# Kernel tuning notes

Measured on AMD Instinct MI355X. Metric: run time of the kernel, lower is better.

## Reference

```python
import jax, jax.numpy as jnp
import numpy as np

B, N, E, D = 128, 100, 100, 64
LAYERS = 2
ALPHA = 0.2  # LeakyReLU negative slope
NEG = -9e15


def leaky_relu(x):
    return jnp.where(x >= 0, x, ALPHA * x)


def setup_inputs() -> dict:
    key = jax.random.key(0)
    ks = jax.random.split(key, 10)
    stdv = 1.0 / np.sqrt(D)
    u = lambda k, shp: jax.random.uniform(k, shp, jnp.float32, -stdv, stdv)
    hidden = jax.random.normal(ks[0], (B, N, D), jnp.float32)
    H = jax.random.randint(ks[1], (B, N, E), 0, 4).astype(jnp.float32)
    s_c = jax.random.normal(ks[2], (B, 1, D), jnp.float32)
    return {
        "hidden": hidden,
        "H": H,
        "s_c": s_c,
        "a10": u(ks[3], (D, 1)),
        "a11": u(ks[4], (D, 1)),
        "a12": u(ks[5], (D, 1)),
        "a20": u(ks[6], (D, 1)),
        "a21": u(ks[7], (D, 1)),
        "a22": u(ks[8], (D, 1)),
    }


def _masked_attn(feat, a0, a1, a2, H, softmax_axis):
    # feat: (B,N,E,D); stack the three attention heads -> (B,N,E,3)
    A = jnp.concatenate([a0, a1, a2], axis=1)  # (D,3)
    atts = leaky_relu(jnp.einsum('bned,dk->bnek', feat, A))
    neg = jnp.full(H.shape, NEG, feat.dtype)
    alpha = jnp.where(H == 1.0, atts[..., 0], neg)
    alpha = jnp.where(H == 2.0, atts[..., 1], alpha)
    alpha = jnp.where(H == 3.0, atts[..., 2], alpha)
    return jax.nn.softmax(alpha, axis=softmax_axis)


def reference(hidden, H, s_c, a10, a11, a12, a20, a21, a22):
    H_adj = (H > 0).astype(hidden.dtype)             # (B,N,E)
    s_c_b = jnp.broadcast_to(s_c, hidden.shape)      # (B,N,D)
    h_emb = hidden
    h_out = jnp.zeros_like(hidden)
    for _ in range(LAYERS):
        # node -> edge attention
        edge_cluster = jnp.einsum('bne,bnd->bed', H_adj, h_emb)        # (B,E,D)
        h_t_cluster = h_emb + s_c_b
        feat = edge_cluster[:, None, :, :] * h_emb[:, :, None, :]       # (B,N,E,D)
        alpha1 = _masked_attn(feat, a10, a11, a12, H, softmax_axis=1)
        edge = jnp.einsum('bne,bnd->bed', alpha1, h_emb)                # (B,E,D)
        # edge -> node attention
        feat_e2n = edge[:, None, :, :] * h_t_cluster[:, :, None, :]     # (B,N,E,D)
        alpha2 = _masked_attn(feat_e2n, a20, a21, a22, H, softmax_axis=2)
        h_emb = jnp.einsum('bne,bed->bnd', alpha2, edge)                # (B,N,D)
        h_out = h_out + h_emb
    return h_out
```

## Files before the change

kernel.cpp:

```cpp
#include <hip/hip_runtime.h>
#include <math.h>

#define B_ 128
#define N_ 100
#define E_ 100
#define D_ 64
#define EH 25
#define LALPHA 0.2f
#define NEGV -9e15f

typedef __attribute__((ext_vector_type(8))) short short8;
typedef __attribute__((ext_vector_type(4))) short short4v;
typedef __attribute__((ext_vector_type(4))) float f32x4;

__device__ __forceinline__ float4 ld4(const float* p) { return *reinterpret_cast<const float4*>(p); }

__device__ __forceinline__ unsigned short f2bf(float x) {
    union { float f; unsigned u; } c; c.f = x;
    return (unsigned short)((c.u + 0x7FFF + ((c.u >> 16) & 1)) >> 16);
}
__device__ __forceinline__ float bf2f(unsigned short h) {
    union { unsigned u; float f; } c; c.u = (unsigned)h << 16;
    return c.f;
}

#define MFMA(a, b, c) __builtin_amdgcn_mfma_f32_16x16x32_bf16((a), (b), (c), 0, 0, 0)

__global__ __launch_bounds__(512, 4) void k_n2e(
    const float* __restrict__ h, const float* __restrict__ Hm,
    const float* __restrict__ a0, const float* __restrict__ a1,
    const float* __restrict__ a2, float* __restrict__ edge)
{
    __shared__ __align__(16) unsigned short hh[112 * 72];
    __shared__ __align__(16) unsigned short hT[64 * 136];
    __shared__ __align__(16) float S[EH * 112];
    __shared__ __align__(16) float ec[32 * 66];
    __shared__ __align__(16) unsigned char kk[112 * 32];
    __shared__ __align__(16) float a_lds[3 * 68];

    unsigned short* m01 = reinterpret_cast<unsigned short*>(S);
    unsigned short* PT  = hh;

    const int b = blockIdx.y, e_base = blockIdx.x * EH;
    const int tid = threadIdx.x;
    const int wv = tid >> 6, ln = tid & 63, l15 = ln & 15, l4 = ln >> 4;

    for (int g = tid; g < 1600; g += 512) {
        const int n = g >> 4, d0 = (g & 15) * 4;
        const float4 v = ld4(&h[(b * N_ + n) * D_ + d0]);
        unsigned short q[4] = { f2bf(v.x), f2bf(v.y), f2bf(v.z), f2bf(v.w) };
        short4v p = { (short)q[0], (short)q[1], (short)q[2], (short)q[3] };
        *reinterpret_cast<short4v*>(&hh[n * 72 + d0]) = p;
        hT[(d0 + 0) * 136 + n] = q[0]; hT[(d0 + 1) * 136 + n] = q[1];
        hT[(d0 + 2) * 136 + n] = q[2]; hT[(d0 + 3) * 136 + n] = q[3];
    }
    for (int i = tid; i < 1536; i += 512) {
        const int n = 100 + (i >> 7), d = i & 127;
        if (d < 72) hh[n * 72 + d] = 0;
    }
    for (int i = tid; i < 4096; i += 512) {
        const int d = i >> 6, c = i & 63;
        if (c < 36) hT[d * 136 + 100 + c] = 0;
    }
    for (int i = tid; i < 544; i += 512) {
        short8 z = { 0,0,0,0,0,0,0,0 };
        reinterpret_cast<short8*>(m01)[i] = z;
    }
    if (tid < 192) {
        const int k = tid >> 6, d = tid & 63;
        a_lds[k * 68 + d] = (k == 0 ? a0 : k == 1 ? a1 : a2)[d];
    }
    __syncthreads();

    for (int i = tid; i < 3584; i += 512) {
        const int n = i >> 5, le = i & 31;
        int v = 0;
        if (n < 100 && le < EH) v = (int)Hm[(b * N_ + n) * E_ + e_base + le];
        kk[n * 32 + le] = (unsigned char)v;
        if (v > 0) m01[le * 136 + n] = 0x3F80;
    }
    __syncthreads();

    {
        const int Mt = wv >> 2, Nt = wv & 3;
        f32x4 acc = { 0,0,0,0 };
        #pragma unroll
        for (int ks = 0; ks < 4; ++ks) {
            const int ko = ks * 32 + l4 * 8;
            short8 af = *reinterpret_cast<const short8*>(&m01[(Mt * 16 + l15) * 136 + ko]);
            short8 bf = *reinterpret_cast<const short8*>(&hT[(Nt * 16 + l15) * 136 + ko]);
            acc = MFMA(af, bf, acc);
        }
        #pragma unroll
        for (int r = 0; r < 4; ++r)
            ec[(Mt * 16 + l4 * 4 + r) * 66 + Nt * 16 + l15] = acc[r];
    }
    __syncthreads();

    {
        const int Mt = wv >> 2, NtB = (wv & 3) * 2;
        const int ntiles = (NtB == 6) ? 1 : 2;
        f32x4 acc[3][2];
        #pragma unroll
        for (int k = 0; k < 3; ++k)
            #pragma unroll
            for (int j = 0; j < 2; ++j) { f32x4 z = { 0,0,0,0 }; acc[k][j] = z; }
        const int arow = Mt * 16 + l15;
        #pragma unroll
        for (int ks = 0; ks < 2; ++ks) {
            const int ko = ks * 32 + l4 * 8;
            short8 bf[2];
            #pragma unroll
            for (int j = 0; j < 2; ++j)
                if (j < ntiles)
                    bf[j] = *reinterpret_cast<const short8*>(&hh[((NtB + j) * 16 + l15) * 72 + ko]);
            float ev[8];
            #pragma unroll
            for (int jj = 0; jj < 8; ++jj) ev[jj] = ec[arow * 66 + ko + jj];
            #pragma unroll
            for (int k = 0; k < 3; ++k) {
                short8 ah, al;
                #pragma unroll
                for (int jj = 0; jj < 8; ++jj) {
                    const float w = ev[jj] * a_lds[k * 68 + ko + jj];
                    const unsigned short hi = f2bf(w);
                    ah[jj] = (short)hi;
                    al[jj] = (short)f2bf(w - bf2f(hi));
                }
                #pragma unroll
                for (int j = 0; j < 2; ++j)
                    if (j < ntiles) {
                        acc[k][j] = MFMA(ah, bf[j], acc[k][j]);
                        acc[k][j] = MFMA(al, bf[j], acc[k][j]);
                    }
            }
        }
        #pragma unroll
        for (int j = 0; j < 2; ++j)
            if (j < ntiles) {
                const int n = (NtB + j) * 16 + l15;
                const int e0 = Mt * 16 + l4 * 4;
                const unsigned kw = *reinterpret_cast<const unsigned*>(&kk[n * 32 + e0]);
                #pragma unroll
                for (int r = 0; r < 4; ++r) {
                    const int er = e0 + r;
                    if (er < EH) {
                        const int kv = (kw >> (8 * r)) & 255;
                        float v = (kv == 1) ? acc[0][j][r] : (kv == 2) ? acc[1][j][r] : acc[2][j][r];
                        v = (v >= 0.f) ? v : LALPHA * v;
                        S[er * 112 + n] = kv ? v : NEGV;
                    }
                }
            }
    }
    __syncthreads();

    {
        const int n1 = ln, n2 = ln + 64;
        #pragma unroll
        for (int t = 0; t < 4; ++t) {
            const int e = wv + 8 * t;
            if (e < EH) {
                const float s1 = S[e * 112 + n1];
                const float s2 = (n2 < 100) ? S[e * 112 + n2] : -INFINITY;
                float mx = fmaxf(s1, s2);
                #pragma unroll
                for (int off = 32; off; off >>= 1) mx = fmaxf(mx, __shfl_xor(mx, off));
                const float p1 = __expf(s1 - mx);
                const float p2 = (n2 < 100) ? __expf(s2 - mx) : 0.f;
                float sum = p1 + p2;
                #pragma unroll
                for (int off = 32; off; off >>= 1) sum += __shfl_xor(sum, off);
                const float inv = 1.f / sum;
                PT[e * 136 + n1] = f2bf(p1 * inv);
                PT[e * 136 + n2] = (n2 < 100) ? f2bf(p2 * inv) : (unsigned short)0;
            }
        }
    }
    __syncthreads();

    {
        const int Mt = wv >> 2, Nt = wv & 3;
        f32x4 acc = { 0,0,0,0 };
        #pragma unroll
        for (int ks = 0; ks < 4; ++ks) {
            const int ko = ks * 32 + l4 * 8;
            short8 af = *reinterpret_cast<const short8*>(&PT[(Mt * 16 + l15) * 136 + ko]);
            short8 bf = *reinterpret_cast<const short8*>(&hT[(Nt * 16 + l15) * 136 + ko]);
            acc = MFMA(af, bf, acc);
        }
        #pragma unroll
        for (int r = 0; r < 4; ++r) {
            const int e = Mt * 16 + l4 * 4 + r;
            if (e < EH)
                edge[(b * E_ + e_base + e) * D_ + Nt * 16 + l15] = acc[r];
        }
    }
}

template <bool WRITE_NEXT, bool ACC>
__global__ __launch_bounds__(512, 4) void k_e2n(
    const float* __restrict__ h, const float* __restrict__ s_c,
    const float* __restrict__ Hm, const float* __restrict__ a0,
    const float* __restrict__ a1, const float* __restrict__ a2,
    const float* __restrict__ edge, float* __restrict__ h_next,
    float* __restrict__ out)
{
    __shared__ __align__(16) unsigned short eh[112 * 72];
    __shared__ __align__(16) unsigned short ehT[64 * 136];
    __shared__ __align__(16) float S2[EH * 112];
    __shared__ __align__(16) float ht[32 * 66];
    __shared__ __align__(16) unsigned char kk2[112 * 32];
    __shared__ __align__(16) float a_lds[3 * 68];

    unsigned short* P2T = eh;

    const int b = blockIdx.y, n_base = blockIdx.x * EH;
    const int tid = threadIdx.x;
    const int wv = tid >> 6, ln = tid & 63, l15 = ln & 15, l4 = ln >> 4;

    for (int g = tid; g < 1600; g += 512) {
        const int e = g >> 4, d0 = (g & 15) * 4;
        const float4 v = ld4(&edge[(b * E_ + e) * D_ + d0]);
        unsigned short q[4] = { f2bf(v.x), f2bf(v.y), f2bf(v.z), f2bf(v.w) };
        short4v p = { (short)q[0], (short)q[1], (short)q[2], (short)q[3] };
        *reinterpret_cast<short4v*>(&eh[e * 72 + d0]) = p;
        ehT[(d0 + 0) * 136 + e] = q[0]; ehT[(d0 + 1) * 136 + e] = q[1];
        ehT[(d0 + 2) * 136 + e] = q[2]; ehT[(d0 + 3) * 136 + e] = q[3];
    }
    for (int i = tid; i < 1536; i += 512) {
        const int e = 100 + (i >> 7), d = i & 127;
        if (d < 72) eh[e * 72 + d] = 0;
    }
    for (int i = tid; i < 4096; i += 512) {
        const int d = i >> 6, c = i & 63;
        if (c < 36) ehT[d * 136 + 100 + c] = 0;
    }
    for (int g = tid; g < 400; g += 512) {
        const int lnn = g >> 4, d0 = (g & 15) * 4;
        const float4 hv = ld4(&h[(b * N_ + n_base + lnn) * D_ + d0]);
        const float4 sc = ld4(&s_c[b * D_ + d0]);
        ht[lnn * 66 + d0 + 0] = hv.x + sc.x;
        ht[lnn * 66 + d0 + 1] = hv.y + sc.y;
        ht[lnn * 66 + d0 + 2] = hv.z + sc.z;
        ht[lnn * 66 + d0 + 3] = hv.w + sc.w;
    }
    for (int i = tid; i < 896; i += 512) {
        const int r = 25 + (i >> 7), c = i & 127;
        if (c < 66) ht[r * 66 + c] = 0.f;
    }
    if (tid < 192) {
        const int k = tid >> 6, d = tid & 63;
        a_lds[k * 68 + d] = (k == 0 ? a0 : k == 1 ? a1 : a2)[d];
    }
    for (int i = tid; i < 3584; i += 512) {
        const int e = i >> 5, lnn = i & 31;
        int v = 0;
        if (e < 100 && lnn < EH) v = (int)Hm[(b * N_ + n_base + lnn) * E_ + e];
        kk2[e * 32 + lnn] = (unsigned char)v;
    }
    __syncthreads();

    {
        const int Mt = wv >> 2, NtB = (wv & 3) * 2;
        const int ntiles = (NtB == 6) ? 1 : 2;
        f32x4 acc[3][2];
        #pragma unroll
        for (int k = 0; k < 3; ++k)
            #pragma unroll
            for (int j = 0; j < 2; ++j) { f32x4 z = { 0,0,0,0 }; acc[k][j] = z; }
        const int arow = Mt * 16 + l15;
        #pragma unroll
        for (int ks = 0; ks < 2; ++ks) {
            const int ko = ks * 32 + l4 * 8;
            short8 bf[2];
            #pragma unroll
            for (int j = 0; j < 2; ++j)
                if (j < ntiles)
                    bf[j] = *reinterpret_cast<const short8*>(&eh[((NtB + j) * 16 + l15) * 72 + ko]);
            float ev[8];
            #pragma unroll
            for (int jj = 0; jj < 8; ++jj) ev[jj] = ht[arow * 66 + ko + jj];
            #pragma unroll
            for (int k = 0; k < 3; ++k) {
                short8 ah, al;
                #pragma unroll
                for (int jj = 0; jj < 8; ++jj) {
                    const float w = ev[jj] * a_lds[k * 68 + ko + jj];
                    const unsigned short hi = f2bf(w);
                    ah[jj] = (short)hi;
                    al[jj] = (short)f2bf(w - bf2f(hi));
                }
                #pragma unroll
                for (int j = 0; j < 2; ++j)
                    if (j < ntiles) {
                        acc[k][j] = MFMA(ah, bf[j], acc[k][j]);
                        acc[k][j] = MFMA(al, bf[j], acc[k][j]);
                    }
            }
        }
        #pragma unroll
        for (int j = 0; j < 2; ++j)
            if (j < ntiles) {
                const int e = (NtB + j) * 16 + l15;
                const int n0 = Mt * 16 + l4 * 4;
                const unsigned kw = *reinterpret_cast<const unsigned*>(&kk2[e * 32 + n0]);
                #pragma unroll
                for (int r = 0; r < 4; ++r) {
                    const int nr = n0 + r;
                    if (nr < EH) {
                        const int kv = (kw >> (8 * r)) & 255;
                        float v = (kv == 1) ? acc[0][j][r] : (kv == 2) ? acc[1][j][r] : acc[2][j][r];
                        v = (v >= 0.f) ? v : LALPHA * v;
                        S2[nr * 112 + e] = kv ? v : NEGV;
                    }
                }
            }
    }
    __syncthreads();

    {
        const int e1 = ln, e2 = ln + 64;
        #pragma unroll
        for (int t = 0; t < 4; ++t) {
            const int nr = wv + 8 * t;
            if (nr < EH) {
                const float s1 = S2[nr * 112 + e1];
                const float s2 = (e2 < 100) ? S2[nr * 112 + e2] : -INFINITY;
                float mx = fmaxf(s1, s2);
                #pragma unroll
                for (int off = 32; off; off >>= 1) mx = fmaxf(mx, __shfl_xor(mx, off));
                const float p1 = __expf(s1 - mx);
                const float p2 = (e2 < 100) ? __expf(s2 - mx) : 0.f;
                float sum = p1 + p2;
                #pragma unroll
                for (int off = 32; off; off >>= 1) sum += __shfl_xor(sum, off);
                const float inv = 1.f / sum;
                P2T[nr * 136 + e1] = f2bf(p1 * inv);
                P2T[nr * 136 + e2] = (e2 < 100) ? f2bf(p2 * inv) : (unsigned short)0;
            }
        }
    }
    __syncthreads();

    {
        const int Mt = wv >> 2, Nt = wv & 3;
        f32x4 acc = { 0,0,0,0 };
        #pragma unroll
        for (int ks = 0; ks < 4; ++ks) {
            const int ko = ks * 32 + l4 * 8;
            short8 af = *reinterpret_cast<const short8*>(&P2T[(Mt * 16 + l15) * 136 + ko]);
            short8 bf = *reinterpret_cast<const short8*>(&ehT[(Nt * 16 + l15) * 136 + ko]);
            acc = MFMA(af, bf, acc);
        }
        #pragma unroll
        for (int r = 0; r < 4; ++r) {
            const int nr = Mt * 16 + l4 * 4 + r;
            if (nr < EH) {
                const int idx = (b * N_ + n_base + nr) * D_ + Nt * 16 + l15;
                const float v = acc[r];
                if (WRITE_NEXT) h_next[idx] = v;
                if (ACC) out[idx] += v; else out[idx] = v;
            }
        }
    }
}

extern "C" void kernel_launch(void* const* d_in, const int* in_sizes, int n_in,
                              void* d_out, int out_size, void* d_ws, size_t ws_size,
                              hipStream_t stream) {
    const float* hidden = (const float*)d_in[0];
    const float* Hm     = (const float*)d_in[1];
    const float* s_c    = (const float*)d_in[2];
    const float* a10    = (const float*)d_in[3];
    const float* a11    = (const float*)d_in[4];
    const float* a12    = (const float*)d_in[5];
    const float* a20    = (const float*)d_in[6];
    const float* a21    = (const float*)d_in[7];
    const float* a22    = (const float*)d_in[8];
    float* out = (float*)d_out;

    float* edge  = (float*)d_ws;
    float* hnext = edge + (size_t)B_ * E_ * D_;

    const dim3 grid(4, B_);

    k_n2e<<<grid, 512, 0, stream>>>(hidden, Hm, a10, a11, a12, edge);
    k_e2n<true, false><<<grid, 512, 0, stream>>>(hidden, s_c, Hm, a20, a21, a22, edge, hnext, out);
    k_n2e<<<grid, 512, 0, stream>>>(hnext, Hm, a10, a11, a12, edge);
    k_e2n<false, true><<<grid, 512, 0, stream>>>(hnext, s_c, Hm, a20, a21, a22, edge, nullptr, out);
}
```

Before: 134.6 us.

## Fuse all four layer kernels into one persistent kernel with per-batch atomic barriers

```diff
diff --git a/kernel.cpp b/kernel.cpp
--- a/kernel.cpp
+++ b/kernel.cpp
@@ -26,343 +26,236 @@
 
 #define MFMA(a, b, c) __builtin_amdgcn_mfma_f32_16x16x32_bf16((a), (b), (c), 0, 0, 0)
 
-__global__ __launch_bounds__(512, 4) void k_n2e(
-    const float* __restrict__ h, const float* __restrict__ Hm,
-    const float* __restrict__ a0, const float* __restrict__ a1,
-    const float* __restrict__ a2, float* __restrict__ edge)
+__global__ __launch_bounds__(512, 4) void k_fused(
+    const float* __restrict__ hidden, const float* __restrict__ Hm,
+    const float* __restrict__ s_c,
+    const float* __restrict__ a10, const float* __restrict__ a11, const float* __restrict__ a12,
+    const float* __restrict__ a20, const float* __restrict__ a21, const float* __restrict__ a22,
+    float* __restrict__ edge, float* __restrict__ hnext, float* __restrict__ out,
+    int* __restrict__ cnt)
 {
     __shared__ __align__(16) unsigned short hh[112 * 72];
     __shared__ __align__(16) unsigned short hT[64 * 136];
-    __shared__ __align__(16) float S[EH * 112];
+    __shared__ __align__(16) unsigned short m01[32 * 136];
+    __shared__ __align__(16) float S[25 * 112];
     __shared__ __align__(16) float ec[32 * 66];
-    __shared__ __align__(16) unsigned char kk[112 * 32];
-    __shared__ __align__(16) float a_lds[3 * 68];
-
-    unsigned short* m01 = reinterpret_cast<unsigned short*>(S);
-    unsigned short* PT  = hh;
-
-    const int b = blockIdx.y, e_base = blockIdx.x * EH;
+    __shared__ unsigned char kkA[112 * 32];
+    __shared__ unsigned char kkB[112 * 32];
+    __shared__ __align__(16) float a_lds[6 * 68];
+
+    const int b = blockIdx.y, q = blockIdx.x;
+    const int e_base = q * EH, n_base = q * EH;
     const int tid = threadIdx.x;
     const int wv = tid >> 6, ln = tid & 63, l15 = ln & 15, l4 = ln >> 4;
 
-    for (int g = tid; g < 1600; g += 512) {
-        const int n = g >> 4, d0 = (g & 15) * 4;
-        const float4 v = ld4(&h[(b * N_ + n) * D_ + d0]);
-        unsigned short q[4] = { f2bf(v.x), f2bf(v.y), f2bf(v.z), f2bf(v.w) };
-        short4v p = { (short)q[0], (short)q[1], (short)q[2], (short)q[3] };
-        *reinterpret_cast<short4v*>(&hh[n * 72 + d0]) = p;
-        hT[(d0 + 0) * 136 + n] = q[0]; hT[(d0 + 1) * 136 + n] = q[1];
-        hT[(d0 + 2) * 136 + n] = q[2]; hT[(d0 + 3) * 136 + n] = q[3];
-    }
-    for (int i = tid; i < 1536; i += 512) {
-        const int n = 100 + (i >> 7), d = i & 127;
-        if (d < 72) hh[n * 72 + d] = 0;
-    }
-    for (int i = tid; i < 4096; i += 512) {
-        const int d = i >> 6, c = i & 63;
-        if (c < 36) hT[d * 136 + 100 + c] = 0;
-    }
-    for (int i = tid; i < 544; i += 512) {
-        short8 z = { 0,0,0,0,0,0,0,0 };
-        reinterpret_cast<short8*>(m01)[i] = z;
-    }
-    if (tid < 192) {
+    auto stage_rows = [&](const float* src) {
+        for (int g = tid; g < 1600; g += 512) {
+            const int r = g >> 4, d0 = (g & 15) * 4;
+            const float4 v = ld4(&src[r * 64 + d0]);
+            const unsigned short q0 = f2bf(v.x), q1 = f2bf(v.y), q2 = f2bf(v.z), q3 = f2bf(v.w);
+            short4v p = { (short)q0, (short)q1, (short)q2, (short)q3 };
+            *reinterpret_cast<short4v*>(&hh[r * 72 + d0]) = p;
+            hT[(d0 + 0) * 136 + r] = q0; hT[(d0 + 1) * 136 + r] = q1;
+            hT[(d0 + 2) * 136 + r] = q2; hT[(d0 + 3) * 136 + r] = q3;
+        }
+    };
+    auto prefill_S = [&]() {
+        for (int i = tid; i < 2800; i += 512) S[i] = NEGV;
+    };
+    auto sync4 = [&](int target) {
+        __threadfence();
+        __syncthreads();
+        if (tid == 0) {
+            atomicAdd(&cnt[b], 1);
+            while (__hip_atomic_load(&cnt[b], __ATOMIC_RELAXED, __HIP_MEMORY_SCOPE_AGENT) < target)
+                __builtin_amdgcn_s_sleep(4);
+            __threadfence();
+        }
+        __syncthreads();
+    };
+    auto score_phase = [&](const unsigned char* kkX, int a_row0) {
+        if (wv < 6) {
+            const int Mt = wv & 1, k = wv >> 1;
+            const int arow = Mt * 16 + l15;
+            f32x4 acc[7];
+            #pragma unroll
+            for (int j = 0; j < 7; ++j) { f32x4 z = { 0,0,0,0 }; acc[j] = z; }
+            #pragma unroll
+            for (int ks = 0; ks < 2; ++ks) {
+                const int ko = ks * 32 + l4 * 8;
+                short8 ah, al;
+                #pragma unroll
+                for (int jj = 0; jj < 8; ++jj) {
+                    const float w = ec[arow * 66 + ko + jj] * a_lds[(a_row0 + k) * 68 + ko + jj];
+                    const unsigned short hi = f2bf(w);
+                    ah[jj] = (short)hi;
+                    al[jj] = (short)f2bf(w - bf2f(hi));
+                }
+                #pragma unroll
+                for (int j = 0; j < 7; ++j) {
+                    const short8 bf = *reinterpret_cast<const short8*>(&hh[(j * 16 + l15) * 72 + ko]);
+                    acc[j] = MFMA(ah, bf, acc[j]);
+                    acc[j] = MFMA(al, bf, acc[j]);
+                }
+            }
+            #pragma unroll
+            for (int j = 0; j < 7; ++j) {
+                const int col = j * 16 + l15;
+                const int r0 = Mt * 16 + l4 * 4;
+                const unsigned kw = *reinterpret_cast<const unsigned*>(&kkX[col * 32 + r0]);
+                #pragma unroll
+                for (int r = 0; r < 4; ++r) {
+                    const int kv = (kw >> (8 * r)) & 255;
+                    if (kv == k + 1) {
+                        float v = acc[j][r];
+                        v = (v >= 0.f) ? v : LALPHA * v;
+                        S[(r0 + r) * 112 + col] = v;
+                    }
+                }
+            }
+        }
+    };
+    auto softmax_phase = [&]() {
+        unsigned short* PT = hh;
+        const int c1 = ln, c2 = ln + 64;
+        #pragma unroll
+        for (int t = 0; t < 4; ++t) {
+            const int r = wv + 8 * t;
+            if (r < EH) {
+                const float s1 = S[r * 112 + c1];
+                const float s2 = (c2 < 100) ? S[r * 112 + c2] : -INFINITY;
+                float mx = fmaxf(s1, s2);
+                #pragma unroll
+                for (int off = 32; off; off >>= 1) mx = fmaxf(mx, __shfl_xor(mx, off));
+                const float p1 = __expf(s1 - mx);
+                const float p2 = (c2 < 100) ? __expf(s2 - mx) : 0.f;
+                float sum = p1 + p2;
+                #pragma unroll
+                for (int off = 32; off; off >>= 1) sum += __shfl_xor(sum, off);
+                const float inv = 1.f / sum;
+                PT[r * 136 + c1] = f2bf(p1 * inv);
+                PT[r * 136 + c2] = (c2 < 100) ? f2bf(p2 * inv) : (unsigned short)0;
+            }
+        }
+    };
+
+    stage_rows(&hidden[(size_t)b * N_ * D_]);
+    for (int i = tid; i < 1536; i += 512) { const int r = 100 + (i >> 7), d = i & 127; if (d < 72) hh[r * 72 + d] = 0; }
+    for (int i = tid; i < 4096; i += 512) { const int d = i >> 6, c = i & 63; if (c < 36) hT[d * 136 + 100 + c] = 0; }
+    for (int i = tid; i < 544; i += 512) { short8 z = { 0,0,0,0,0,0,0,0 }; reinterpret_cast<short8*>(m01)[i] = z; }
+    if (tid < 384) {
         const int k = tid >> 6, d = tid & 63;
-        a_lds[k * 68 + d] = (k == 0 ? a0 : k == 1 ? a1 : a2)[d];
+        const float* ap = (k == 0) ? a10 : (k == 1) ? a11 : (k == 2) ? a12 : (k == 3) ? a20 : (k == 4) ? a21 : a22;
+        a_lds[k * 68 + d] = ap[d];
     }
     __syncthreads();
-
     for (int i = tid; i < 3584; i += 512) {
         const int n = i >> 5, le = i & 31;
         int v = 0;
-        if (n < 100 && le < EH) v = (int)Hm[(b * N_ + n) * E_ + e_base + le];
-        kk[n * 32 + le] = (unsigned char)v;
+        if (n < 100 && le < EH) v = (int)Hm[((size_t)b * N_ + n) * E_ + e_base + le];
+        kkA[n * 32 + le] = (unsigned char)v;
         if (v > 0) m01[le * 136 + n] = 0x3F80;
-    }
-    __syncthreads();
-
-    {
-        const int Mt = wv >> 2, Nt = wv & 3;
-        f32x4 acc = { 0,0,0,0 };
-        #pragma unroll
-        for (int ks = 0; ks < 4; ++ks) {
-            const int ko = ks * 32 + l4 * 8;
-            short8 af = *reinterpret_cast<const short8*>(&m01[(Mt * 16 + l15) * 136 + ko]);
-            short8 bf = *reinterpret_cast<const short8*>(&hT[(Nt * 16 + l15) * 136 + ko]);
-            acc = MFMA(af, bf, acc);
-        }
-        #pragma unroll
-        for (int r = 0; r < 4; ++r)
-            ec[(Mt * 16 + l4 * 4 + r) * 66 + Nt * 16 + l15] = acc[r];
-    }
-    __syncthreads();
-
-    {
-        const int Mt = wv >> 2, NtB = (wv & 3) * 2;
-        const int ntiles = (NtB == 6) ? 1 : 2;
-        f32x4 acc[3][2];
-        #pragma unroll
-        for (int k = 0; k < 3; ++k)
-            #pragma unroll
-            for (int j = 0; j < 2; ++j) { f32x4 z = { 0,0,0,0 }; acc[k][j] = z; }
-        const int arow = Mt * 16 + l15;
-        #pragma unroll
-        for (int ks = 0; ks < 2; ++ks) {
-            const int ko = ks * 32 + l4 * 8;
-            short8 bf[2];
-            #pragma unroll
-            for (int j = 0; j < 2; ++j)
-                if (j < ntiles)
-                    bf[j] = *reinterpret_cast<const short8*>(&hh[((NtB + j) * 16 + l15) * 72 + ko]);
-            float ev[8];
-            #pragma unroll
-            for (int jj = 0; jj < 8; ++jj) ev[jj] = ec[arow * 66 + ko + jj];
-            #pragma unroll
-            for (int k = 0; k < 3; ++k) {
-                short8 ah, al;
-                #pragma unroll
-                for (int jj = 0; jj < 8; ++jj) {
-                    const float w = ev[jj] * a_lds[k * 68 + ko + jj];
-                    const unsigned short hi = f2bf(w);
-                    ah[jj] = (short)hi;
-                    al[jj] = (short)f2bf(w - bf2f(hi));
-                }
-                #pragma unroll
-                for (int j = 0; j < 2; ++j)
-                    if (j < ntiles) {
-                        acc[k][j] = MFMA(ah, bf[j], acc[k][j]);
-                        acc[k][j] = MFMA(al, bf[j], acc[k][j]);
-                    }
-            }
-        }
-        #pragma unroll
-        for (int j = 0; j < 2; ++j)
-            if (j < ntiles) {
-                const int n = (NtB + j) * 16 + l15;
-                const int e0 = Mt * 16 + l4 * 4;
-                const unsigned kw = *reinterpret_cast<const unsigned*>(&kk[n * 32 + e0]);
-                #pragma unroll
-                for (int r = 0; r < 4; ++r) {
-                    const int er = e0 + r;
-                    if (er < EH) {
-                        const int kv = (kw >> (8 * r)) & 255;
-                        float v = (kv == 1) ? acc[0][j][r] : (kv == 2) ? acc[1][j][r] : acc[2][j][r];
-                        v = (v >= 0.f) ? v : LALPHA * v;
-                        S[er * 112 + n] = kv ? v : NEGV;
-                    }
-                }
-            }
-    }
-    __syncthreads();
-
-    {
-        const int n1 = ln, n2 = ln + 64;
-        #pragma unroll
-        for (int t = 0; t < 4; ++t) {
-            const int e = wv + 8 * t;
-            if (e < EH) {
-                const float s1 = S[e * 112 + n1];
-                const float s2 = (n2 < 100) ? S[e * 112 + n2] : -INFINITY;
-                float mx = fmaxf(s1, s2);
-                #pragma unroll
-                for (int off = 32; off; off >>= 1) mx = fmaxf(mx, __shfl_xor(mx, off));
-                const float p1 = __expf(s1 - mx);
-                const float p2 = (n2 < 100) ? __expf(s2 - mx) : 0.f;
-                float sum = p1 + p2;
-                #pragma unroll
-                for (int off = 32; off; off >>= 1) sum += __shfl_xor(sum, off);
-                const float inv = 1.f / sum;
-                PT[e * 136 + n1] = f2bf(p1 * inv);
-                PT[e * 136 + n2] = (n2 < 100) ? f2bf(p2 * inv) : (unsigned short)0;
-            }
-        }
-    }
-    __syncthreads();
-
-    {
-        const int Mt = wv >> 2, Nt = wv & 3;
-        f32x4 acc = { 0,0,0,0 };
-        #pragma unroll
-        for (int ks = 0; ks < 4; ++ks) {
-            const int ko = ks * 32 + l4 * 8;
-            short8 af = *reinterpret_cast<const short8*>(&PT[(Mt * 16 + l15) * 136 + ko]);
-            short8 bf = *reinterpret_cast<const short8*>(&hT[(Nt * 16 + l15) * 136 + ko]);
-            acc = MFMA(af, bf, acc);
-        }
-        #pragma unroll
-        for (int r = 0; r < 4; ++r) {
-            const int e = Mt * 16 + l4 * 4 + r;
-            if (e < EH)
-                edge[(b * E_ + e_base + e) * D_ + Nt * 16 + l15] = acc[r];
-        }
-    }
-}
-
-template <bool WRITE_NEXT, bool ACC>
-__global__ __launch_bounds__(512, 4) void k_e2n(
-    const float* __restrict__ h, const float* __restrict__ s_c,
-    const float* __restrict__ Hm, const float* __restrict__ a0,
-    const float* __restrict__ a1, const float* __restrict__ a2,
-    const float* __restrict__ edge, float* __restrict__ h_next,
-    float* __restrict__ out)
-{
-    __shared__ __align__(16) unsigned short eh[112 * 72];
-    __shared__ __align__(16) unsigned short ehT[64 * 136];
-    __shared__ __align__(16) float S2[EH * 112];
-    __shared__ __align__(16) float ht[32 * 66];
-    __shared__ __align__(16) unsigned char kk2[112 * 32];
-    __shared__ __align__(16) float a_lds[3 * 68];
-
-    unsigned short* P2T = eh;
-
-    const int b = blockIdx.y, n_base = blockIdx.x * EH;
-    const int tid = threadIdx.x;
-    const int wv = tid >> 6, ln = tid & 63, l15 = ln & 15, l4 = ln >> 4;
-
-    for (int g = tid; g < 1600; g += 512) {
-        const int e = g >> 4, d0 = (g & 15) * 4;
-        const float4 v = ld4(&edge[(b * E_ + e) * D_ + d0]);
-        unsigned short q[4] = { f2bf(v.x), f2bf(v.y), f2bf(v.z), f2bf(v.w) };
-        short4v p = { (short)q[0], (short)q[1], (short)q[2], (short)q[3] };
-        *reinterpret_cast<short4v*>(&eh[e * 72 + d0]) = p;
-        ehT[(d0 + 0) * 136 + e] = q[0]; ehT[(d0 + 1) * 136 + e] = q[1];
-        ehT[(d0 + 2) * 136 + e] = q[2]; ehT[(d0 + 3) * 136 + e] = q[3];
-    }
-    for (int i = tid; i < 1536; i += 512) {
-        const int e = 100 + (i >> 7), d = i & 127;
-        if (d < 72) eh[e * 72 + d] = 0;
-    }
-    for (int i = tid; i < 4096; i += 512) {
-        const int d = i >> 6, c = i & 63;
-        if (c < 36) ehT[d * 136 + 100 + c] = 0;
-    }
-    for (int g = tid; g < 400; g += 512) {
-        const int lnn = g >> 4, d0 = (g & 15) * 4;
-        const float4 hv = ld4(&h[(b * N_ + n_base + lnn) * D_ + d0]);
-        const float4 sc = ld4(&s_c[b * D_ + d0]);
-        ht[lnn * 66 + d0 + 0] = hv.x + sc.x;
-        ht[lnn * 66 + d0 + 1] = hv.y + sc.y;
-        ht[lnn * 66 + d0 + 2] = hv.z + sc.z;
-        ht[lnn * 66 + d0 + 3] = hv.w + sc.w;
-    }
-    for (int i = tid; i < 896; i += 512) {
-        const int r = 25 + (i >> 7), c = i & 127;
-        if (c < 66) ht[r * 66 + c] = 0.f;
-    }
-    if (tid < 192) {
-        const int k = tid >> 6, d = tid & 63;
-        a_lds[k * 68 + d] = (k == 0 ? a0 : k == 1 ? a1 : a2)[d];
     }
     for (int i = tid; i < 3584; i += 512) {
         const int e = i >> 5, lnn = i & 31;
         int v = 0;
-        if (e < 100 && lnn < EH) v = (int)Hm[(b * N_ + n_base + lnn) * E_ + e];
-        kk2[e * 32 + lnn] = (unsigned char)v;
-    }
+        if (e < 100 && lnn < EH) v = (int)Hm[((size_t)b * N_ + n_base + lnn) * E_ + e];
+        kkB[e * 32 + lnn] = (unsigned char)v;
+    }
+    prefill_S();
     __syncthreads();
 
-    {
-        const int Mt = wv >> 2, NtB = (wv & 3) * 2;
-        const int ntiles = (NtB == 6) ? 1 : 2;
-        f32x4 acc[3][2];
-        #pragma unroll
-        for (int k = 0; k < 3; ++k)
-            #pragma unroll
-            for (int j = 0; j < 2; ++j) { f32x4 z = { 0,0,0,0 }; acc[k][j] = z; }
-        const int arow = Mt * 16 + l15;
-        #pragma unroll
-        for (int ks = 0; ks < 2; ++ks) {
-            const int ko = ks * 32 + l4 * 8;
-            short8 bf[2];
-            #pragma unroll
-            for (int j = 0; j < 2; ++j)
-                if (j < ntiles)
-                    bf[j] = *reinterpret_cast<const short8*>(&eh[((NtB + j) * 16 + l15) * 72 + ko]);
-            float ev[8];
-            #pragma unroll
-            for (int jj = 0; jj < 8; ++jj) ev[jj] = ht[arow * 66 + ko + jj];
-            #pragma unroll
-            for (int k = 0; k < 3; ++k) {
-                short8 ah, al;
-                #pragma unroll
-                for (int jj = 0; jj < 8; ++jj) {
-                    const float w = ev[jj] * a_lds[k * 68 + ko + jj];
-                    const unsigned short hi = f2bf(w);
-                    ah[jj] = (short)hi;
-                    al[jj] = (short)f2bf(w - bf2f(hi));
-                }
-                #pragma unroll
-                for (int j = 0; j < 2; ++j)
-                    if (j < ntiles) {
-                        acc[k][j] = MFMA(ah, bf[j], acc[k][j]);
-                        acc[k][j] = MFMA(al, bf[j], acc[k][j]);
-                    }
-            }
-        }
-        #pragma unroll
-        for (int j = 0; j < 2; ++j)
-            if (j < ntiles) {
-                const int e = (NtB + j) * 16 + l15;
-                const int n0 = Mt * 16 + l4 * 4;
-                const unsigned kw = *reinterpret_cast<const unsigned*>(&kk2[e * 32 + n0]);
+    f32x4 racc = { 0,0,0,0 };
+    for (int layer = 0; layer < 2; ++layer) {
+        const float* hsrc = layer ? hnext : hidden;
+        if (layer == 1) {
+            stage_rows(&hnext[(size_t)b * N_ * D_]);
+            prefill_S();
+            __syncthreads();
+        }
+        {
+            const int Mt = wv >> 2, Nt = wv & 3;
+            f32x4 acc = { 0,0,0,0 };
+            #pragma unroll
+            for (int ks = 0; ks < 4; ++ks) {
+                const int ko = ks * 32 + l4 * 8;
+                const short8 af = *reinterpret_cast<const short8*>(&m01[(Mt * 16 + l15) * 136 + ko]);
+                const short8 bf = *reinterpret_cast<const short8*>(&hT[(Nt * 16 + l15) * 136 + ko]);
+                acc = MFMA(af, bf, acc);
+            }
+            #pragma unroll
+            for (int r = 0; r < 4; ++r)
+                ec[(Mt * 16 + l4 * 4 + r) * 66 + Nt * 16 + l15] = acc[r];
+        }
+        __syncthreads();
+        score_phase(kkA, 0);
+        __syncthreads();
+        softmax_phase();
+        __syncthreads();
+        {
+            const unsigned short* PT = hh;
+            const int Mt = wv >> 2, Nt = wv & 3;
+            f32x4 acc = { 0,0,0,0 };
+            #pragma unroll
+            for (int ks = 0; ks < 4; ++ks) {
+                const int ko = ks * 32 + l4 * 8;
+                const short8 af = *reinterpret_cast<const short8*>(&PT[(Mt * 16 + l15) * 136 + ko]);
+                const short8 bf = *reinterpret_cast<const short8*>(&hT[(Nt * 16 + l15) * 136 + ko]);
+                acc = MFMA(af, bf, acc);
+            }
+            #pragma unroll
+            for (int r = 0; r < 4; ++r) {
+                const int e = Mt * 16 + l4 * 4 + r;
+                if (e < EH) edge[((size_t)b * E_ + e_base + e) * D_ + Nt * 16 + l15] = acc[r];
+            }
+        }
+        sync4(layer * 8 + 4);
+
+        stage_rows(&edge[(size_t)b * E_ * D_]);
+        for (int g = tid; g < 400; g += 512) {
+            const int lnn = g >> 4, d0 = (g & 15) * 4;
+            const float4 hv = ld4(&hsrc[((size_t)b * N_ + n_base + lnn) * D_ + d0]);
+            const float4 sc = ld4(&s_c[(size_t)b * D_ + d0]);
+            ec[lnn * 66 + d0 + 0] = hv.x + sc.x;
+            ec[lnn * 66 + d0 + 1] = hv.y + sc.y;
+            ec[lnn * 66 + d0 + 2] = hv.z + sc.z;
+            ec[lnn * 66 + d0 + 3] = hv.w + sc.w;
+        }
+        prefill_S();
+        __syncthreads();
+        score_phase(kkB, 3);
+        __syncthreads();
+        softmax_phase();
+        __syncthreads();
+        {
+            const unsigned short* P2T = hh;
+            const int Mt = wv >> 2, Nt = wv & 3;
+            f32x4 acc = { 0,0,0,0 };
+            #pragma unroll
+            for (int ks = 0; ks < 4; ++ks) {
+                const int ko = ks * 32 + l4 * 8;
+                const short8 af = *reinterpret_cast<const short8*>(&P2T[(Mt * 16 + l15) * 136 + ko]);
+                const short8 bf = *reinterpret_cast<const short8*>(&hT[(Nt * 16 + l15) * 136 + ko]);
+                acc = MFMA(af, bf, acc);
+            }
+            if (layer == 0) {
                 #pragma unroll
                 for (int r = 0; r < 4; ++r) {
-                    const int nr = n0 + r;
-                    if (nr < EH) {
-                        const int kv = (kw >> (8 * r)) & 255;
-                        float v = (kv == 1) ? acc[0][j][r] : (kv == 2) ? acc[1][j][r] : acc[2][j][r];
-                        v = (v >= 0.f) ? v : LALPHA * v;
-                        S2[nr * 112 + e] = kv ? v : NEGV;
-                    }
-                }
-            }
-    }
-    __syncthreads();
-
-    {
-        const int e1 = ln, e2 = ln + 64;
-        #pragma unroll
-        for (int t = 0; t < 4; ++t) {
-            const int nr = wv + 8 * t;
-            if (nr < EH) {
-                const float s1 = S2[nr * 112 + e1];
-                const float s2 = (e2 < 100) ? S2[nr * 112 + e2] : -INFINITY;
-                float mx = fmaxf(s1, s2);
-                #pragma unroll
-                for (int off = 32; off; off >>= 1) mx = fmaxf(mx, __shfl_xor(mx, off));
-                const float p1 = __expf(s1 - mx);
-                const float p2 = (e2 < 100) ? __expf(s2 - mx) : 0.f;
-                float sum = p1 + p2;
-                #pragma unroll
-                for (int off = 32; off; off >>= 1) sum += __shfl_xor(sum, off);
-                const float inv = 1.f / sum;
-                P2T[nr * 136 + e1] = f2bf(p1 * inv);
-                P2T[nr * 136 + e2] = (e2 < 100) ? f2bf(p2 * inv) : (unsigned short)0;
-            }
-        }
-    }
-    __syncthreads();
-
-    {
-        const int Mt = wv >> 2, Nt = wv & 3;
-        f32x4 acc = { 0,0,0,0 };
-        #pragma unroll
-        for (int ks = 0; ks < 4; ++ks) {
-            const int ko = ks * 32 + l4 * 8;
-            short8 af = *reinterpret_cast<const short8*>(&P2T[(Mt * 16 + l15) * 136 + ko]);
-            short8 bf = *reinterpret_cast<const short8*>(&ehT[(Nt * 16 + l15) * 136 + ko]);
-            acc = MFMA(af, bf, acc);
-        }
-        #pragma unroll
-        for (int r = 0; r < 4; ++r) {
-            const int nr = Mt * 16 + l4 * 4 + r;
-            if (nr < EH) {
-                const int idx = (b * N_ + n_base + nr) * D_ + Nt * 16 + l15;
-                const float v = acc[r];
-                if (WRITE_NEXT) h_next[idx] = v;
-                if (ACC) out[idx] += v; else out[idx] = v;
-            }
-        }
+                    const int nr = Mt * 16 + l4 * 4 + r;
+                    if (nr < EH)
+                        hnext[((size_t)b * N_ + n_base + nr) * D_ + Nt * 16 + l15] = acc[r];
+                }
+                racc = acc;
+            } else {
+                #pragma unroll
+                for (int r = 0; r < 4; ++r) {
+                    const int nr = Mt * 16 + l4 * 4 + r;
+                    if (nr < EH)
+                        out[((size_t)b * N_ + n_base + nr) * D_ + Nt * 16 + l15] = racc[r] + acc[r];
+                }
+            }
+        }
+        if (layer == 0) sync4(8);
     }
 }
 
@@ -382,11 +275,10 @@
 
     float* edge  = (float*)d_ws;
     float* hnext = edge + (size_t)B_ * E_ * D_;
-
-    const dim3 grid(4, B_);
-
-    k_n2e<<<grid, 512, 0, stream>>>(hidden, Hm, a10, a11, a12, edge);
-    k_e2n<true, false><<<grid, 512, 0, stream>>>(hidden, s_c, Hm, a20, a21, a22, edge, hnext, out);
-    k_n2e<<<grid, 512, 0, stream>>>(hnext, Hm, a10, a11, a12, edge);
-    k_e2n<false, true><<<grid, 512, 0, stream>>>(hnext, s_c, Hm, a20, a21, a22, edge, nullptr, out);
-}
+    int*   cnt   = (int*)(hnext + (size_t)B_ * N_ * D_);
+
+    hipMemsetAsync(cnt, 0, B_ * sizeof(int), stream);
+    k_fused<<<dim3(4, B_), 512, 0, stream>>>(hidden, Hm, s_c,
+                                             a10, a11, a12, a20, a21, a22,
+                                             edge, hnext, out, cnt);
+}
```

Measured after the change: 424.1 us. 3.15x slower.
